# Performance work log

Hardware: AMD Instinct MI355X
Metric: run time of the kernel (lower is better)

## Reference

```python
import jax, jax.numpy as jnp
import numpy as np

# Tap offsets (dy, dx) within the 3x3 footprint for each kernel_type.
# kernel_type 0 -> 5-tap skeleton (center + 4-neighbors), 1 -> full 3x3, else -> 3-tap row.
TAPS = {
    0: [(1, 1), (0, 1), (1, 0), (1, 2), (2, 1)],
    1: [(i, j) for i in range(3) for j in range(3)],
    2: [(1, 0), (1, 1), (1, 2)],
}

KERNEL_TYPE = 0
STRIDE = 1
PAD = 1
DIL = 1
SPATIAL = False


def setup_inputs() -> dict:
    key = jax.random.key(0)
    k1, k2 = jax.random.split(key)
    N, Ci, H, W = 16, 256, 64, 64
    Co, K = 256, len(TAPS[KERNEL_TYPE])
    x = jax.random.normal(k1, (N, Ci, H, W), dtype=jnp.float32)
    # kaiming-uniform-ish scale
    bound = np.sqrt(6.0 / (Ci * K))
    weight = jax.random.uniform(k2, (Co, Ci, K), dtype=jnp.float32, minval=-bound, maxval=bound)
    return {"x": x, "weight": weight, "step": 0}


def _spatial_conv(x, weight):
    # x: [N, Ci, H, W], weight: [Co, Ci, K]
    taps = TAPS[KERNEL_TYPE]
    N, Ci, H, W = x.shape
    Hout = (H + 2 * PAD - (DIL * 2 + 1)) // STRIDE + 1
    Wout = (W + 2 * PAD - (DIL * 2 + 1)) // STRIDE + 1
    xp = jnp.pad(x, ((0, 0), (0, 0), (PAD, PAD), (PAD, PAD)))
    outs = []
    for k, (dy, dx) in enumerate(taps):
        y0, x0 = dy * DIL, dx * DIL
        xs = xp[:, :, y0:y0 + (Hout - 1) * STRIDE + 1:STRIDE,
                      x0:x0 + (Wout - 1) * STRIDE + 1:STRIDE]  # [N, Ci, Hout, Wout]
        outs.append(jnp.einsum('nchw,oc->nohw', xs, weight[:, :, k]))
    return jnp.stack(outs, axis=0)  # [K, N, Co, Hout, Wout]


def reference(x, weight, step):
    out = _spatial_conv(x, weight)  # [K, N, Co, H, W]
    if SPATIAL:
        K, N, Co, Ho, Wo = out.shape
        out = jnp.transpose(out, (1, 0, 2, 3, 4)).reshape(N, K * Co, Ho, Wo)
    else:
        out = out.sum(axis=0)  # sum over taps -> [N, Co, H, W]
    return out
```

## Files before the change

### kernel.cpp

```cpp
#include <hip/hip_runtime.h>
#include <hip/hip_bf16.h>
#include <cstddef>

#define N_  16
#define CI  256
#define CO  256
#define KT  5

typedef __attribute__((ext_vector_type(8)))  short  short8;
typedef __attribute__((ext_vector_type(8)))  unsigned short ushort8;
typedef __attribute__((ext_vector_type(4)))  unsigned int uint4v;
typedef __attribute__((ext_vector_type(16))) float  floatx16;

static __device__ __forceinline__ unsigned short f2bf(float f) {
    union { float f; unsigned u; } v; v.f = f;
    unsigned r = v.u + 0x7fff + ((v.u >> 16) & 1);
    return (unsigned short)(r >> 16);
}

__global__ void wtrans_kernel(const float* __restrict__ w, unsigned short* __restrict__ wb) {
    int idx = blockIdx.x * 256 + threadIdx.x;
    if (idx >= KT * CO * CI) return;
    int e  = idx & 7;
    int o  = (idx >> 3) & 255;
    int lh = (idx >> 11) & 1;
    int ks = (idx >> 12) & 1;
    int c  = (idx >> 13) & 7;
    int k  = idx >> 16;
    int ci = c * 32 + ks * 16 + lh * 8 + e;
    wb[idx] = f2bf(w[(size_t)o * (CI * KT) + ci * KT + k]);
}

__global__ __launch_bounds__(512, 4) void conv_mfma(const float* __restrict__ x,
                                                    const unsigned short* __restrict__ wb,
                                                    float* __restrict__ out) {
    __shared__ ushort8 lds[2112];

    const int tid = threadIdx.x;
    const int bx0 = blockIdx.x;
    const int bx  = (bx0 & 7) * 64 + (bx0 >> 3);
    const int g   = bx & 31;
    const int n   = bx >> 5;
    const int h0  = g * 2;

    const int lane  = tid & 63;
    const int wv    = tid >> 6;
    const int l31   = lane & 31;
    const int lh    = lane >> 5;
    const int owave = (wv & 3) * 64;
    const int hrow  = wv >> 2;

    const int sw  = tid & 63;
    const int scg = (tid >> 6) & 3;
    const int sr2 = tid >> 8;

    if (tid < 64) {
        int buf = tid & 1;
        int wp  = ((tid >> 1) & 1) * 65;
        int cg  = (tid >> 2) & 3;
        int r   = (tid >> 4) & 3;
        lds[buf * 1056 + r * 264 + cg * 66 + wp] = (ushort8)0;
    }

    const float* xn = x + (size_t)n * CI * 4096;

    float xr[2][8];
    auto load_chunk = [&](int c) {
        #pragma unroll
        for (int ii = 0; ii < 2; ++ii) {
            const int i  = sr2 * 2 + ii;
            const int hh = h0 - 1 + i;
            if ((unsigned)hh < 64u) {
                const float* p = xn + (c * 32 + scg * 8) * 4096 + hh * 64 + sw;
                #pragma unroll
                for (int e = 0; e < 8; ++e) xr[ii][e] = p[e * 4096];
            } else {
                #pragma unroll
                for (int e = 0; e < 8; ++e) xr[ii][e] = 0.f;
            }
        }
    };
    auto write_chunk = [&](int b) {
        #pragma unroll
        for (int ii = 0; ii < 2; ++ii) {
            const int i = sr2 * 2 + ii;
            uint4v v;
            #pragma unroll
            for (int e = 0; e < 4; ++e) {
                __hip_bfloat162 pk = __float22bfloat162_rn(
                    make_float2(xr[ii][2 * e], xr[ii][2 * e + 1]));
                union { __hip_bfloat162 h; unsigned u; } cv; cv.h = pk;
                v[e] = cv.u;
            }
            *(uint4v*)&lds[b * 1056 + i * 264 + scg * 66 + (sw + 1)] = v;
        }
    };

    floatx16 acc[2][2];
    #pragma unroll
    for (int ot = 0; ot < 2; ++ot)
        #pragma unroll
        for (int t = 0; t < 2; ++t)
            #pragma unroll
            for (int e = 0; e < 16; ++e) acc[ot][t][e] = 0.f;

    const char* ldsb = (const char*)lds + (hrow * 4224 + lh * 1056 + l31 * 16);
    const unsigned short* wA = wb + lh * 2048 + (owave + l31) * 8;

    load_chunk(0);
    write_chunk(0);
    __syncthreads();

    for (int c = 0; c < 8; ++c) {
        const char* bufb = ldsb + (c & 1) * 16896;
        const unsigned short* wc = wA + c * 8192;

        #pragma unroll
        for (int ks = 0; ks < 2; ++ks) {
            #pragma unroll
            for (int k = 0; k < KT; ++k) {
                const int dy = (k == 1) ? 0 : (k == 4) ? 2 : 1;
                const int dx = (k == 2) ? 0 : (k == 3) ? 2 : 1;
                const short8 a0 = *(const short8*)(wc + k * 65536 + ks * 4096);
                const short8 a1 = *(const short8*)(wc + k * 65536 + ks * 4096 + 256);
                const short8 b0 = *(const short8*)(bufb + (dy * 264 + ks * 132 + dx) * 16);
                const short8 b1 = *(const short8*)(bufb + (dy * 264 + ks * 132 + 32 + dx) * 16);
                acc[0][0] = __builtin_amdgcn_mfma_f32_32x32x16_bf16(a0, b0, acc[0][0], 0, 0, 0);
                acc[1][0] = __builtin_amdgcn_mfma_f32_32x32x16_bf16(a1, b0, acc[1][0], 0, 0, 0);
                acc[0][1] = __builtin_amdgcn_mfma_f32_32x32x16_bf16(a0, b1, acc[0][1], 0, 0, 0);
                acc[1][1] = __builtin_amdgcn_mfma_f32_32x32x16_bf16(a1, b1, acc[1][1], 0, 0, 0);
            }
            if (ks == 0 && c < 7) load_chunk(c + 1);
        }

        if (c < 7) write_chunk((c + 1) & 1);
        __syncthreads();
    }

    const int h = h0 + hrow;
    #pragma unroll
    for (int ot = 0; ot < 2; ++ot) {
        #pragma unroll
        for (int wh = 0; wh < 2; ++wh) {
            #pragma unroll
            for (int reg = 0; reg < 16; ++reg) {
                int o = owave + ot * 32 + (reg & 3) + 8 * (reg >> 2) + 4 * lh;
                out[(((size_t)n * CO + o) * 64 + h) * 64 + wh * 32 + l31] = acc[ot][wh][reg];
            }
        }
    }
}

extern "C" void kernel_launch(void* const* d_in, const int* in_sizes, int n_in,
                              void* d_out, int out_size, void* d_ws, size_t ws_size,
                              hipStream_t stream) {
    const float* x = (const float*)d_in[0];
    const float* w = (const float*)d_in[1];
    float* out = (float*)d_out;

    unsigned short* wb = (unsigned short*)d_ws;

    wtrans_kernel<<<dim3((KT * CO * CI + 255) / 256), dim3(256), 0, stream>>>(w, wb);
    conv_mfma<<<dim3(N_ * 32), dim3(512), 0, stream>>>(x, wb, out);
}
```

Measured before the change: 151.5 us.

## Stage weights into LDS via async global_load_lds with half-chunk pipelining

Weight fragments for the MFMA A operand are now copied into double-buffered LDS with direct global-to-LDS loads, where before each wave read them from global memory. The main loop is split into two half-chunk phases, each ending in a hand-placed barrier and waitcnt, so the next weight half and the next input chunk load while the current half computes. Out-of-range halo rows are handled by clamping the row index and multiplying by a zero mask, which removes the branch. The larger dynamic shared memory (about 113 KB) lowers the launch bound to 2 blocks per CU, trading occupancy for reuse and overlap.

Result: no change. 148.7 us (-1.9%).

```diff
diff --git a/kernel.cpp b/kernel.cpp
--- a/kernel.cpp
+++ b/kernel.cpp
@@ -7,6 +7,11 @@
 #define CO  256
 #define KT  5
 
+#define XBUF_B   16896
+#define WOFF     33792
+#define WBUF_B   40960
+#define SMEM_B   115712
+
 typedef __attribute__((ext_vector_type(8)))  short  short8;
 typedef __attribute__((ext_vector_type(8)))  unsigned short ushort8;
 typedef __attribute__((ext_vector_type(4)))  unsigned int uint4v;
@@ -16,6 +21,12 @@
     union { float f; unsigned u; } v; v.f = f;
     unsigned r = v.u + 0x7fff + ((v.u >> 16) & 1);
     return (unsigned short)(r >> 16);
+}
+
+typedef const __attribute__((address_space(1))) unsigned int g_u32;
+typedef __attribute__((address_space(3))) unsigned int l_u32;
+static __device__ __forceinline__ void gload_lds16(const void* g, void* l) {
+    __builtin_amdgcn_global_load_lds((g_u32*)g, (l_u32*)l, 16, 0, 0);
 }
 
 __global__ void wtrans_kernel(const float* __restrict__ w, unsigned short* __restrict__ wb) {
@@ -31,10 +42,28 @@
     wb[idx] = f2bf(w[(size_t)o * (CI * KT) + ci * KT + k]);
 }
 
-__global__ __launch_bounds__(512, 4) void conv_mfma(const float* __restrict__ x,
+template<int KS>
+static __device__ __forceinline__ void compute_half(const char* wB, const char* xB,
+                                                    floatx16 (&acc)[2][2]) {
+    #pragma unroll
+    for (int k = 0; k < KT; ++k) {
+        const int dy = (k == 1) ? 0 : (k == 4) ? 2 : 1;
+        const int dx = (k == 2) ? 0 : (k == 3) ? 2 : 1;
+        const short8 a0 = *(const short8*)(wB + k * 8192);
+        const short8 a1 = *(const short8*)(wB + k * 8192 + 512);
+        const short8 b0 = *(const short8*)(xB + (dy * 264 + KS * 132 + dx) * 16);
+        const short8 b1 = *(const short8*)(xB + (dy * 264 + KS * 132 + 32 + dx) * 16);
+        acc[0][0] = __builtin_amdgcn_mfma_f32_32x32x16_bf16(a0, b0, acc[0][0], 0, 0, 0);
+        acc[1][0] = __builtin_amdgcn_mfma_f32_32x32x16_bf16(a1, b0, acc[1][0], 0, 0, 0);
+        acc[0][1] = __builtin_amdgcn_mfma_f32_32x32x16_bf16(a0, b1, acc[0][1], 0, 0, 0);
+        acc[1][1] = __builtin_amdgcn_mfma_f32_32x32x16_bf16(a1, b1, acc[1][1], 0, 0, 0);
+    }
+}
+
+__global__ __launch_bounds__(512, 2) void conv_mfma(const float* __restrict__ x,
                                                     const unsigned short* __restrict__ wb,
                                                     float* __restrict__ out) {
-    __shared__ ushort8 lds[2112];
+    extern __shared__ char smem[];
 
     const int tid = threadIdx.x;
     const int bx0 = blockIdx.x;
@@ -59,25 +88,27 @@
         int wp  = ((tid >> 1) & 1) * 65;
         int cg  = (tid >> 2) & 3;
         int r   = (tid >> 4) & 3;
-        lds[buf * 1056 + r * 264 + cg * 66 + wp] = (ushort8)0;
+        ((ushort8*)smem)[buf * 1056 + r * 264 + cg * 66 + wp] = (ushort8)0;
     }
 
     const float* xn = x + (size_t)n * CI * 4096;
+
+    float zm[2];
+    int   hcl[2];
+    #pragma unroll
+    for (int ii = 0; ii < 2; ++ii) {
+        int hh = h0 - 1 + sr2 * 2 + ii;
+        zm[ii]  = ((unsigned)hh < 64u) ? 1.f : 0.f;
+        hcl[ii] = hh < 0 ? 0 : (hh > 63 ? 63 : hh);
+    }
 
     float xr[2][8];
     auto load_chunk = [&](int c) {
         #pragma unroll
         for (int ii = 0; ii < 2; ++ii) {
-            const int i  = sr2 * 2 + ii;
-            const int hh = h0 - 1 + i;
-            if ((unsigned)hh < 64u) {
-                const float* p = xn + (c * 32 + scg * 8) * 4096 + hh * 64 + sw;
-                #pragma unroll
-                for (int e = 0; e < 8; ++e) xr[ii][e] = p[e * 4096];
-            } else {
-                #pragma unroll
-                for (int e = 0; e < 8; ++e) xr[ii][e] = 0.f;
-            }
+            const float* p = xn + (c * 32 + scg * 8) * 4096 + hcl[ii] * 64 + sw;
+            #pragma unroll
+            for (int e = 0; e < 8; ++e) xr[ii][e] = p[e * 4096];
         }
     };
     auto write_chunk = [&](int b) {
@@ -88,13 +119,20 @@
             #pragma unroll
             for (int e = 0; e < 4; ++e) {
                 __hip_bfloat162 pk = __float22bfloat162_rn(
-                    make_float2(xr[ii][2 * e], xr[ii][2 * e + 1]));
+                    make_float2(zm[ii] * xr[ii][2 * e], zm[ii] * xr[ii][2 * e + 1]));
                 union { __hip_bfloat162 h; unsigned u; } cv; cv.h = pk;
                 v[e] = cv.u;
             }
-            *(uint4v*)&lds[b * 1056 + i * 264 + scg * 66 + (sw + 1)] = v;
+            *(uint4v*)&((ushort8*)smem)[b * 1056 + i * 264 + scg * 66 + (sw + 1)] = v;
         }
     };
+    auto stage_w = [&](int c, int ks, int buf) {
+        const char* src = (const char*)wb + c * 16384 + ks * 8192 + wv * 1024 + lane * 16;
+        char* dst = smem + WOFF + buf * WBUF_B + wv * 1024;
+        #pragma unroll
+        for (int i = 0; i < 5; ++i)
+            gload_lds16(src + (size_t)i * 131072, dst + i * 8192);
+    };
 
     floatx16 acc[2][2];
     #pragma unroll
@@ -104,37 +142,42 @@
             #pragma unroll
             for (int e = 0; e < 16; ++e) acc[ot][t][e] = 0.f;
 
-    const char* ldsb = (const char*)lds + (hrow * 4224 + lh * 1056 + l31 * 16);
-    const unsigned short* wA = wb + lh * 2048 + (owave + l31) * 8;
-
+    const char* xbase = smem + hrow * 4224 + lh * 1056 + l31 * 16;
+    const char* wbase = smem + WOFF + lh * 4096 + (owave + l31) * 16;
+
+    stage_w(0, 0, 0);
     load_chunk(0);
     write_chunk(0);
-    __syncthreads();
+    __builtin_amdgcn_sched_barrier(0);
+    asm volatile("s_waitcnt vmcnt(0) lgkmcnt(0)" ::: "memory");
+    __builtin_amdgcn_s_barrier();
+    __builtin_amdgcn_sched_barrier(0);
 
     for (int c = 0; c < 8; ++c) {
-        const char* bufb = ldsb + (c & 1) * 16896;
-        const unsigned short* wc = wA + c * 8192;
-
-        #pragma unroll
-        for (int ks = 0; ks < 2; ++ks) {
-            #pragma unroll
-            for (int k = 0; k < KT; ++k) {
-                const int dy = (k == 1) ? 0 : (k == 4) ? 2 : 1;
-                const int dx = (k == 2) ? 0 : (k == 3) ? 2 : 1;
-                const short8 a0 = *(const short8*)(wc + k * 65536 + ks * 4096);
-                const short8 a1 = *(const short8*)(wc + k * 65536 + ks * 4096 + 256);
-                const short8 b0 = *(const short8*)(bufb + (dy * 264 + ks * 132 + dx) * 16);
-                const short8 b1 = *(const short8*)(bufb + (dy * 264 + ks * 132 + 32 + dx) * 16);
-                acc[0][0] = __builtin_amdgcn_mfma_f32_32x32x16_bf16(a0, b0, acc[0][0], 0, 0, 0);
-                acc[1][0] = __builtin_amdgcn_mfma_f32_32x32x16_bf16(a1, b0, acc[1][0], 0, 0, 0);
-                acc[0][1] = __builtin_amdgcn_mfma_f32_32x32x16_bf16(a0, b1, acc[0][1], 0, 0, 0);
-                acc[1][1] = __builtin_amdgcn_mfma_f32_32x32x16_bf16(a1, b1, acc[1][1], 0, 0, 0);
-            }
-            if (ks == 0 && c < 7) load_chunk(c + 1);
-        }
-
+        const char* xb = xbase + (c & 1) * XBUF_B;
+
+        stage_w(c, 1, 1);
+        asm volatile("" ::: "memory");
+        if (c < 7) load_chunk(c + 1);
+        asm volatile("" ::: "memory");
+        compute_half<0>(wbase, xb, acc);
+        __builtin_amdgcn_sched_barrier(0);
+        if (c < 7) asm volatile("s_waitcnt vmcnt(16) lgkmcnt(0)" ::: "memory");
+        else       asm volatile("s_waitcnt vmcnt(0) lgkmcnt(0)"  ::: "memory");
+        __builtin_amdgcn_s_barrier();
+        __builtin_amdgcn_sched_barrier(0);
+
+        if (c < 7) stage_w(c + 1, 0, 0);
+        asm volatile("" ::: "memory");
         if (c < 7) write_chunk((c + 1) & 1);
-        __syncthreads();
+        asm volatile("" ::: "memory");
+        compute_half<1>(wbase + WBUF_B, xb, acc);
+        __builtin_amdgcn_sched_barrier(0);
+        if (c < 7) {
+            asm volatile("s_waitcnt vmcnt(0) lgkmcnt(0)" ::: "memory");
+            __builtin_amdgcn_s_barrier();
+            __builtin_amdgcn_sched_barrier(0);
+        }
     }
 
     const int h = h0 + hrow;
@@ -160,6 +203,13 @@
 
     unsigned short* wb = (unsigned short*)d_ws;
 
+    static bool attr_set = false;
+    if (!attr_set) {
+        hipFuncSetAttribute(reinterpret_cast<const void*>(conv_mfma),
+                            hipFuncAttributeMaxDynamicSharedMemorySize, SMEM_B);
+        attr_set = true;
+    }
+
     wtrans_kernel<<<dim3((KT * CO * CI + 255) / 256), dim3(256), 0, stream>>>(w, wb);
-    conv_mfma<<<dim3(N_ * 32), dim3(512), 0, stream>>>(x, wb, out);
-}
+    conv_mfma<<<dim3(N_ * 32), dim3(512), SMEM_B, stream>>>(x, wb, out);
+}
```
